# Optimization experiments

Hardware: AMD Instinct MI355X
Metric: run time of the kernel (lower is better)

The kernel has to match this reference:

```python
import jax, jax.numpy as jnp
import numpy as np

IMAGE_MAX_DIM = 1024
POOL = 7
NUM_CLASSES = 81
N_ROIS = 2000
BN_EPS = 1e-3


def _make_boxes(key, n):
    k1, k2, k3, k4 = jax.random.split(key, 4)
    cx = jax.random.uniform(k1, (n,), minval=0.0, maxval=IMAGE_MAX_DIM)
    cy = jax.random.uniform(k2, (n,), minval=0.0, maxval=IMAGE_MAX_DIM)
    w = jax.random.uniform(k3, (n,), minval=16.0, maxval=512.0)
    h = jax.random.uniform(k4, (n,), minval=16.0, maxval=512.0)
    x1 = jnp.clip(cx - w / 2, 0.0, IMAGE_MAX_DIM - 2.0)
    y1 = jnp.clip(cy - h / 2, 0.0, IMAGE_MAX_DIM - 2.0)
    x2 = jnp.clip(cx + w / 2, x1 + 1.0, IMAGE_MAX_DIM)
    y2 = jnp.clip(cy + h / 2, y1 + 1.0, IMAGE_MAX_DIM)
    return jnp.stack([x1, y1, x2, y2], axis=-1)[None]  # [1, n, 4]


def setup_inputs() -> dict:
    key = jax.random.key(0)
    ks = jax.random.split(key, 16)
    d = {
        'p2': jax.random.normal(ks[0], (1, 256, 256, 256), jnp.float32),
        'p3': jax.random.normal(ks[1], (1, 256, 128, 128), jnp.float32),
        'p4': jax.random.normal(ks[2], (1, 256, 64, 64), jnp.float32),
        'p5': jax.random.normal(ks[3], (1, 256, 32, 32), jnp.float32),
        'rpn_rois': _make_boxes(ks[4], N_ROIS),
        'conv1_w': jax.random.normal(ks[5], (1024, 256, POOL, POOL), jnp.float32) * 0.02,
        'conv1_b': jnp.zeros((1024,), jnp.float32),
        'bn1_g': jnp.ones((1024,), jnp.float32),
        'bn1_b': jnp.zeros((1024,), jnp.float32),
        'bn1_m': jnp.zeros((1024,), jnp.float32),
        'bn1_v': jnp.ones((1024,), jnp.float32),
        'conv2_w': jax.random.normal(ks[6], (1024, 1024), jnp.float32) * 0.02,
        'conv2_b': jnp.zeros((1024,), jnp.float32),
        'bn2_g': jnp.ones((1024,), jnp.float32),
        'bn2_b': jnp.zeros((1024,), jnp.float32),
        'bn2_m': jnp.zeros((1024,), jnp.float32),
        'bn2_v': jnp.ones((1024,), jnp.float32),
        'logits_w': jax.random.normal(ks[7], (NUM_CLASSES, 1024), jnp.float32) * 0.02,
        'logits_b': jnp.zeros((NUM_CLASSES,), jnp.float32),
        'bbox_w': jax.random.normal(ks[8], (NUM_CLASSES * 4, 1024), jnp.float32) * 0.02,
        'bbox_b': jnp.zeros((NUM_CLASSES * 4,), jnp.float32),
    }
    return d


def _crop_resize(fmap, boxes):
    """TF-style crop_and_resize, bilinear. fmap [C,H,W]; boxes [N,4] = (y1,x1,y2,x2) normalized."""
    C, H, W = fmap.shape
    dt = fmap.dtype
    y1, x1, y2, x2 = boxes[:, 0], boxes[:, 1], boxes[:, 2], boxes[:, 3]
    t = (jnp.arange(POOL, dtype=dt) / (POOL - 1))  # [P]
    ys = y1[:, None] * (H - 1) + t[None, :] * ((y2 - y1) * (H - 1))[:, None]  # [N,P]
    xs = x1[:, None] * (W - 1) + t[None, :] * ((x2 - x1) * (W - 1))[:, None]  # [N,P]
    y0 = jnp.floor(ys)
    x0 = jnp.floor(xs)
    ly = (ys - y0)[None, :, :, None]  # [1,N,P,1]
    lx = (xs - x0)[None, :, None, :]  # [1,N,1,P]
    y0i = jnp.clip(y0.astype(jnp.int32), 0, H - 1)
    y1i = jnp.clip(y0i + 1, 0, H - 1)
    x0i = jnp.clip(x0.astype(jnp.int32), 0, W - 1)
    x1i = jnp.clip(x0i + 1, 0, W - 1)

    def g(yi, xi):  # -> [C,N,P,P]
        return fmap[:, yi[:, :, None], xi[:, None, :]]

    out = (g(y0i, x0i) * (1 - ly) * (1 - lx) + g(y0i, x1i) * (1 - ly) * lx
           + g(y1i, x0i) * ly * (1 - lx) + g(y1i, x1i) * ly * lx)
    return jnp.transpose(out, (1, 0, 2, 3))  # [N,C,P,P]


def _forward(p2, p3, p4, p5, rpn_rois, conv1_w, conv1_b, bn1_g, bn1_b, bn1_m, bn1_v,
             conv2_w, conv2_b, bn2_g, bn2_b, bn2_m, bn2_v, logits_w, logits_b, bbox_w, bbox_b):
    rois = rpn_rois.reshape(-1, 4)  # [N,4] (x1,y1,x2,y2) in pixels
    x1, y1, x2, y2 = rois[:, 0], rois[:, 1], rois[:, 2], rois[:, 3]
    # level = clamp(round(log2(sqrt(area)/224)) + 4, 2, 5)
    roi_level = jnp.clip(jnp.round(jnp.log2(jnp.sqrt((y2 - y1) * (x2 - x1)) / 224.0)) + 4.0, 2.0, 5.0)
    boxes_n = (rois / float(IMAGE_MAX_DIM))[:, [1, 0, 3, 2]]  # (y1,x1,y2,x2) normalized

    pooled = jnp.zeros((rois.shape[0], 256, POOL, POOL), rois.dtype)
    for lvl, fmap in zip(range(2, 6), [p2, p3, p4, p5]):
        crops = _crop_resize(fmap[0], boxes_n)  # [N,256,P,P]
        mask = (roi_level == float(lvl))[:, None, None, None]
        pooled = pooled + jnp.where(mask, crops, 0.0)

    # conv1: 7x7 valid conv over [N,256,7,7] -> [N,1024]
    h = jnp.einsum('nchw,ochw->no', pooled, conv1_w) + conv1_b
    h = (h - bn1_m) * jax.lax.rsqrt(bn1_v + BN_EPS) * bn1_g + bn1_b
    h = jax.nn.relu(h)
    # conv2: 1x1 conv == matmul
    h = h @ conv2_w.T + conv2_b
    h = (h - bn2_m) * jax.lax.rsqrt(bn2_v + BN_EPS) * bn2_g + bn2_b
    shared = jax.nn.relu(h)  # [N,1024]

    logits = shared @ logits_w.T + logits_b
    probs = jax.nn.softmax(logits, axis=-1)
    bbox = shared @ bbox_w.T + bbox_b
    return (logits.reshape(1, N_ROIS, NUM_CLASSES),
            probs.reshape(1, N_ROIS, NUM_CLASSES),
            bbox.reshape(1, N_ROIS, NUM_CLASSES, 4))


def reference(p2, p3, p4, p5, rpn_rois, conv1_w, conv1_b, bn1_g, bn1_b, bn1_m, bn1_v,
              conv2_w, conv2_b, bn2_g, bn2_b, bn2_m, bn2_v, logits_w, logits_b, bbox_w, bbox_b):
    return _forward(p2, p3, p4, p5, rpn_rois, conv1_w, conv1_b, bn1_g, bn1_b, bn1_m, bn1_v,
                    conv2_w, conv2_b, bn2_g, bn2_b, bn2_m, bn2_v, logits_w, logits_b, bbox_w, bbox_b)
```

## Files before the change

### kernel.cpp

```cpp
#include <hip/hip_runtime.h>
#include <stdint.h>

#define NROI 2000
#define MPAD 2048
#define KP   12544
#define N1   1024
#define NCLS 81
#define NBOX 324
#define N3   405
#define N3P  448
#define BN_EPS 0.001f
#define KSPLIT 8

typedef __attribute__((ext_vector_type(8))) short bf16x8;
typedef __attribute__((ext_vector_type(4))) float f32x4;
typedef __attribute__((ext_vector_type(8))) unsigned short u16x8;

__device__ inline unsigned short f2bf(float f) {
  union { float f; unsigned u; } v; v.f = f;
  unsigned r = v.u + 0x7fffu + ((v.u >> 16) & 1u);
  return (unsigned short)(r >> 16);
}

__device__ inline float bf2f(unsigned short h) {
  union { unsigned u; float f; } v; v.u = (unsigned)h << 16; return v.f;
}

__device__ inline void gld16(const unsigned short* g, unsigned short* l) {
  __builtin_amdgcn_global_load_lds(
      (const __attribute__((address_space(1))) void*)g,
      (__attribute__((address_space(3))) void*)l, 16, 0, 0);
}

__device__ __forceinline__ void kslice(int kz, int& off, int& len) {
  if (kz < 4) { off = kz * 1536; len = 1536; }
  else        { off = 6144 + (kz - 4) * 1600; len = 1600; }
}

__global__ __launch_bounds__(256) void front_t(
    const float* __restrict__ p2, const float* __restrict__ p3,
    const float* __restrict__ p4, const float* __restrict__ p5,
    unsigned short* __restrict__ f2t, unsigned short* __restrict__ f3t,
    unsigned short* __restrict__ f4t, unsigned short* __restrict__ f5t) {
  int bb2 = blockIdx.x;
  int t = threadIdx.x;
  const float* src;
  unsigned short* dst;
  int HW;
  if (bb2 < 1024)      { src = p2; dst = f2t; HW = 65536; }
  else if (bb2 < 1280) { bb2 -= 1024; src = p3; dst = f3t; HW = 16384; }
  else if (bb2 < 1344) { bb2 -= 1280; src = p4; dst = f4t; HW = 4096; }
  else                 { bb2 -= 1344; src = p5; dst = f5t; HW = 1024; }
  int p0 = bb2 * 64;
  int lane = t & 63, w = t >> 6;
  int pq = (lane & 15) * 4;
  int cg = (lane >> 4) * 8;
#pragma unroll
  for (int it = 0; it < 2; ++it) {
    int c = w * 64 + it * 32 + cg;
    const float* sp = src + (size_t)c * HW + p0 + pq;
    float4 v[8];
#pragma unroll
    for (int k = 0; k < 8; ++k)
      v[k] = *(const float4*)(sp + (size_t)k * HW);
    unsigned short* dp = dst + (size_t)(p0 + pq) * 256 + c;
    u16x8 o0, o1, o2, o3;
#pragma unroll
    for (int k = 0; k < 8; ++k) {
      o0[k] = f2bf(v[k].x);
      o1[k] = f2bf(v[k].y);
      o2[k] = f2bf(v[k].z);
      o3[k] = f2bf(v[k].w);
    }
    *(u16x8*)(dp)       = o0;
    *(u16x8*)(dp + 256) = o1;
    *(u16x8*)(dp + 512) = o2;
    *(u16x8*)(dp + 768) = o3;
  }
}

__global__ __launch_bounds__(256) void roi_prep(
    const unsigned short* __restrict__ f2t, const unsigned short* __restrict__ f3t,
    const unsigned short* __restrict__ f4t, const unsigned short* __restrict__ f5t,
    const float* __restrict__ rois, unsigned short* __restrict__ pooled,
    const float* __restrict__ c1w, const float* __restrict__ c2w,
    const float* __restrict__ lw, const float* __restrict__ bw,
    const float* c1b, const float* g1, const float* b1, const float* m1, const float* v1,
    const float* c2b, const float* g2, const float* b2, const float* m2, const float* v2,
    const float* lb, const float* bb,
    unsigned short* __restrict__ w1p, unsigned short* __restrict__ w2b,
    unsigned short* __restrict__ w3b,
    float* s1, float* t1, float* s2, float* t2, float* b3) {
  __shared__ unsigned short srep[6272];
  int b = blockIdx.x;
  int t = threadIdx.x;
  if (b < 2048) {
    int n = b;
    int lane = t & 63, w = t >> 6;
    int c0 = lane * 4;
    unsigned short* out = pooled + (size_t)n * KP;
    if (n >= NROI) {
      for (int p = w; p < 49; p += 4)
        *(ushort4*)(out + p * 256 + c0) = make_ushort4(0, 0, 0, 0);
      return;
    }
    float x1 = rois[n * 4 + 0], y1 = rois[n * 4 + 1];
    float x2 = rois[n * 4 + 2], y2 = rois[n * 4 + 3];
    float area = (y2 - y1) * (x2 - x1);
    float lvl_f = rintf(log2f(sqrtf(area) / 224.0f)) + 4.0f;
    lvl_f = fminf(fmaxf(lvl_f, 2.0f), 5.0f);
    int lvl = (int)lvl_f;
    const unsigned short* f;
    int H;
    if (lvl == 2)      { f = f2t; H = 256; }
    else if (lvl == 3) { f = f3t; H = 128; }
    else if (lvl == 4) { f = f4t; H = 64;  }
    else               { f = f5t; H = 32;  }
    int W = H;
    const float inv = 1.0f / 1024.0f;
    float yn1 = y1 * inv, xn1 = x1 * inv, yn2 = y2 * inv, xn2 = x2 * inv;
    float hs = (yn2 - yn1) * (H - 1);
    float ws = (xn2 - xn1) * (W - 1);
    float yb = yn1 * (H - 1);
    float xb = xn1 * (W - 1);

    for (int p = w; p < 49; p += 4) {
      int py = p / 7, px = p - py * 7;
      float ysv = yb + ((float)py / 6.0f) * hs;
      float xsv = xb + ((float)px / 6.0f) * ws;
      float y0f = floorf(ysv), x0f = floorf(xsv);
      float ly = ysv - y0f, lx = xsv - x0f;
      int y0 = min(max((int)y0f, 0), H - 1);
      int y1i = min(y0 + 1, H - 1);
      int x0 = min(max((int)x0f, 0), W - 1);
      int x1i = min(x0 + 1, W - 1);
      ushort4 v00 = *(const ushort4*)(f + ((size_t)y0 * W + x0) * 256 + c0);
      ushort4 v01 = *(const ushort4*)(f + ((size_t)y0 * W + x1i) * 256 + c0);
      ushort4 v10 = *(const ushort4*)(f + ((size_t)y1i * W + x0) * 256 + c0);
      ushort4 v11 = *(const ushort4*)(f + ((size_t)y1i * W + x1i) * 256 + c0);
      ushort4 o;
      {
        float a = bf2f(v00.x), bq = bf2f(v01.x), cq = bf2f(v10.x), d = bf2f(v11.x);
        float top = a + lx * (bq - a), bot = cq + lx * (d - cq);
        o.x = f2bf(top + ly * (bot - top));
      }
      {
        float a = bf2f(v00.y), bq = bf2f(v01.y), cq = bf2f(v10.y), d = bf2f(v11.y);
        float top = a + lx * (bq - a), bot = cq + lx * (d - cq);
        o.y = f2bf(top + ly * (bot - top));
      }
      {
        float a = bf2f(v00.z), bq = bf2f(v01.z), cq = bf2f(v10.z), d = bf2f(v11.z);
        float top = a + lx * (bq - a), bot = cq + lx * (d - cq);
        o.z = f2bf(top + ly * (bot - top));
      }
      {
        float a = bf2f(v00.w), bq = bf2f(v01.w), cq = bf2f(v10.w), d = bf2f(v11.w);
        float top = a + lx * (bq - a), bot = cq + lx * (d - cq);
        o.w = f2bf(top + ly * (bot - top));
      }
      *(ushort4*)(out + p * 256 + c0) = o;
    }
  } else if (b < 4096) {
    int idx = b - 2048;
    int o = idx >> 1, h = idx & 1;
    const float4* src = (const float4*)(c1w + (size_t)o * KP + h * 6272);
    for (int k = t; k < 1568; k += 256) {
      float4 v = src[k];
      ushort4 q;
      q.x = f2bf(v.x); q.y = f2bf(v.y); q.z = f2bf(v.z); q.w = f2bf(v.w);
      *(ushort4*)&srep[k * 4] = q;
    }
    __syncthreads();
    unsigned short* dst = w1p + (size_t)o * KP + h * 128;
    int ch4 = (t & 31) * 4;
    int jw = t >> 5;
    for (int j = jw; j < 49; j += 8) {
      ushort4 q;
      q.x = srep[(ch4 + 0) * 49 + j];
      q.y = srep[(ch4 + 1) * 49 + j];
      q.z = srep[(ch4 + 2) * 49 + j];
      q.w = srep[(ch4 + 3) * 49 + j];
      *(ushort4*)(dst + j * 256 + ch4) = q;
    }
  } else if (b < 5120) {
    int j4 = (b - 4096) * 256 + t;
    float4 v = ((const float4*)c2w)[j4];
    ushort4 q;
    q.x = f2bf(v.x); q.y = f2bf(v.y); q.z = f2bf(v.z); q.w = f2bf(v.w);
    *(ushort4*)(w2b + (size_t)j4 * 4) = q;
  } else if (b < 5568) {
    int row = b - 5120;
    int k = t * 4;
    float4 v = {0.f, 0.f, 0.f, 0.f};
    if (row < NCLS)      v = *(const float4*)(lw + (size_t)row * 1024 + k);
    else if (row < N3)   v = *(const float4*)(bw + (size_t)(row - NCLS) * 1024 + k);
    ushort4 q;
    q.x = f2bf(v.x); q.y = f2bf(v.y); q.z = f2bf(v.z); q.w = f2bf(v.w);
    *(ushort4*)(w3b + (size_t)row * 1024 + k) = q;
  } else {
    for (int i = t; i < 1024; i += 256) {
      float sc = g1[i] * rsqrtf(v1[i] + BN_EPS);
      s1[i] = sc;
      t1[i] = (c1b[i] - m1[i]) * sc + b1[i];
      float ss = g2[i] * rsqrtf(v2[i] + BN_EPS);
      s2[i] = ss;
      t2[i] = (c2b[i] - m2[i]) * ss + b2[i];
    }
    for (int i = t; i < N3P; i += 256)
      b3[i] = (i < NCLS) ? lb[i] : (i < N3 ? bb[i - NCLS] : 0.0f);
  }
}

__global__ __launch_bounds__(512, 2) void gemm1_sk2(
    const unsigned short* __restrict__ A, const unsigned short* __restrict__ B,
    unsigned short* __restrict__ part) {
  __shared__ unsigned short AsF[4 * 8192];
  __shared__ unsigned short BsF[4 * 8192];
  int bid = blockIdx.x;
  int kz = bid & 7;
  int u = bid >> 3;
  int bn0 = (u & 3) * 256;
  int bm0 = (u >> 2) * 256;
  int koff, klen;
  kslice(kz, koff, klen);
  int nt = klen >> 6;

  int t = threadIdx.x;
  int lane = t & 63, w = t >> 6;
  int wr = w >> 2, wc = w & 3;
  int ln = lane & 15, q = lane >> 4;

  int clog = (lane & 3) ^ ((lane >> 3) & 3);
  int l4 = lane >> 2;
  const unsigned short* gA0 = A + (size_t)(bm0 + w * 32 + l4) * KP + koff + clog * 8;
  const unsigned short* gA1 = gA0 + (size_t)16 * KP;
  const unsigned short* gB0 = B + (size_t)(bn0 + w * 32 + l4) * KP + koff + clog * 8;
  const unsigned short* gB1 = gB0 + (size_t)16 * KP;
  int dc0 = (w * 128 + lane) * 8;
  int dc1 = dc0 + 64 * 8;

  int rxor = (q ^ ((ln >> 1) & 3)) * 8;
  int rdA = (wr * 128 + ln) * 32 + rxor;
  int rdB = (wc * 64 + ln) * 32 + rxor;

  f32x4 acc[8][4] = {};

#pragma unroll
  for (int kk = 0; kk < 2; ++kk) {
    int src = kk * 32;
    int db = kk * 8192;
    gld16(gA0 + src, AsF + db + dc0);
    gld16(gA1 + src, AsF + db + dc1);
    gld16(gB0 + src, BsF + db + dc0);
    gld16(gB1 + src, BsF + db + dc1);
  }
  asm volatile("s_waitcnt vmcnt(4)" ::: "memory");
  __builtin_amdgcn_s_barrier();
  asm volatile("" ::: "memory");

  for (int tt = 0; tt < nt; ++tt) {
    int slot = tt & 1;
    int nslot = slot ^ 1;
    int knext = (tt + 1 < nt) ? (tt + 1) * 64 : 0;
#pragma unroll
    for (int kk = 0; kk < 2; ++kk) {
      int rb = (slot * 2 + kk) * 8192;
      bf16x8 af[8], bfr[4];
#pragma unroll
      for (int mi = 0; mi < 8; ++mi)
        af[mi] = *(const bf16x8*)&AsF[rb + rdA + mi * 512];
#pragma unroll
      for (int nj = 0; nj < 4; ++nj)
        bfr[nj] = *(const bf16x8*)&BsF[rb + rdB + nj * 512];

      int src = knext + kk * 32;
      int db = (nslot * 2 + kk) * 8192;
      gld16(gA0 + src, AsF + db + dc0);
      gld16(gA1 + src, AsF + db + dc1);
      gld16(gB0 + src, BsF + db + dc0);
      gld16(gB1 + src, BsF + db + dc1);

      asm volatile("s_waitcnt vmcnt(4)" ::: "memory");
      __builtin_amdgcn_s_barrier();
      asm volatile("" ::: "memory");

      __builtin_amdgcn_s_setprio(1);
#pragma unroll
      for (int mi = 0; mi < 8; ++mi)
#pragma unroll
        for (int nj = 0; nj < 4; ++nj)
          acc[mi][nj] = __builtin_amdgcn_mfma_f32_16x16x32_bf16(
              af[mi], bfr[nj], acc[mi][nj], 0, 0, 0);
      __builtin_amdgcn_s_setprio(0);

      asm volatile("" ::: "memory");
      __builtin_amdgcn_s_barrier();
      asm volatile("" ::: "memory");
    }
  }

  unsigned short* po = part + (size_t)kz * MPAD * N1;
#pragma unroll
  for (int mi = 0; mi < 8; ++mi) {
    int m = bm0 + wr * 128 + mi * 16 + q * 4;
#pragma unroll
    for (int nj = 0; nj < 4; ++nj) {
      int n = bn0 + wc * 64 + nj * 16 + ln;
#pragma unroll
      for (int r = 0; r < 4; ++r)
        po[(size_t)(m + r) * N1 + n] = f2bf(acc[mi][nj][r]);
    }
  }
}

__global__ void reduce_sk(const unsigned short* __restrict__ part,
                          const float* __restrict__ sc, const float* __restrict__ sh,
                          unsigned short* __restrict__ outb) {
  const size_t P = (size_t)MPAD * N1;
  int m = blockIdx.x;
  int t = threadIdx.x;
  float4 v = {0.f, 0.f, 0.f, 0.f};
#pragma unroll
  for (int kz = 0; kz < KSPLIT; ++kz) {
    ushort4 u = *(const ushort4*)(part + kz * P + (size_t)m * N1 + t * 4);
    v.x += bf2f(u.x); v.y += bf2f(u.y); v.z += bf2f(u.z); v.w += bf2f(u.w);
  }
  int n0 = t * 4;
  ushort4 o;
  if (m < NROI) {
    o.x = f2bf(fmaxf(v.x * sc[n0 + 0] + sh[n0 + 0], 0.0f));
    o.y = f2bf(fmaxf(v.y * sc[n0 + 1] + sh[n0 + 1], 0.0f));
    o.z = f2bf(fmaxf(v.z * sc[n0 + 2] + sh[n0 + 2], 0.0f));
    o.w = f2bf(fmaxf(v.w * sc[n0 + 3] + sh[n0 + 3], 0.0f));
  } else {
    o = make_ushort4(0, 0, 0, 0);
  }
  *(ushort4*)(outb + (size_t)m * N1 + n0) = o;
}

template <int MODE>
__global__ __launch_bounds__(256) void gemm_bt(
    const unsigned short* __restrict__ A, const unsigned short* __restrict__ B,
    int M, int N, int K,
    const float* __restrict__ sc, const float* __restrict__ sh,
    unsigned short* __restrict__ outb, float* __restrict__ outf,
    int validM, int ldo) {
  __shared__ unsigned short As[64 * 64];
  __shared__ unsigned short Bs[64 * 64];
  int bm0 = blockIdx.y * 64;
  int bn0 = blockIdx.x * 64;
  int t = threadIdx.x;
  int lane = t & 63, w = t >> 6;
  int wm = (w & 1) * 32, wn = (w >> 1) * 32;
  int ln = lane & 15, q = lane >> 4;

  int r8 = t >> 3, j8 = t & 7;
  int sj = j8 ^ (r8 & 7);
  const unsigned short* ga = A + (size_t)(bm0 + r8) * K + sj * 8;
  const unsigned short* gb = B + (size_t)(bn0 + r8) * K + sj * 8;
  unsigned short* la = &As[t * 8];
  unsigned short* lb = &Bs[t * 8];
  int e = ln & 7;

  f32x4 acc00 = {0.f, 0.f, 0.f, 0.f}, acc01 = {0.f, 0.f, 0.f, 0.f};
  f32x4 acc10 = {0.f, 0.f, 0.f, 0.f}, acc11 = {0.f, 0.f, 0.f, 0.f};

  for (int k0 = 0; k0 < K; k0 += 64) {
    gld16(ga + k0, la);
    gld16(ga + k0 + (size_t)32 * K, la + 2048);
    gld16(gb + k0, lb);
    gld16(gb + k0 + (size_t)32 * K, lb + 2048);
    __syncthreads();
#pragma unroll
    for (int h = 0; h < 2; ++h) {
      int slot = ((h * 4 + q) ^ e) * 8;
      bf16x8 a0 = *(const bf16x8*)&As[(wm + ln) * 64 + slot];
      bf16x8 a1 = *(const bf16x8*)&As[(wm + 16 + ln) * 64 + slot];
      bf16x8 b0 = *(const bf16x8*)&Bs[(wn + ln) * 64 + slot];
      bf16x8 b1 = *(const bf16x8*)&Bs[(wn + 16 + ln) * 64 + slot];
      acc00 = __builtin_amdgcn_mfma_f32_16x16x32_bf16(a0, b0, acc00, 0, 0, 0);
      acc01 = __builtin_amdgcn_mfma_f32_16x16x32_bf16(a0, b1, acc01, 0, 0, 0);
      acc10 = __builtin_amdgcn_mfma_f32_16x16x32_bf16(a1, b0, acc10, 0, 0, 0);
      acc11 = __builtin_amdgcn_mfma_f32_16x16x32_bf16(a1, b1, acc11, 0, 0, 0);
    }
    __syncthreads();
  }

  f32x4 accs[2][2] = {{acc00, acc01}, {acc10, acc11}};
#pragma unroll
  for (int i = 0; i < 2; ++i)
#pragma unroll
    for (int j = 0; j < 2; ++j)
#pragma unroll
      for (int r = 0; r < 4; ++r) {
        int m = bm0 + wm + i * 16 + q * 4 + r;
        int n = bn0 + wn + j * 16 + ln;
        float v = accs[i][j][r];
        if (MODE == 1) {
          float o = fmaxf(v * sc[n] + sh[n], 0.0f);
          outb[(size_t)m * ldo + n] = (m < validM) ? f2bf(o) : (unsigned short)0;
        } else {
          outf[(size_t)m * ldo + n] = v + sh[n];
        }
      }
}

__global__ void head(const float* __restrict__ fc3, float* __restrict__ out) {
  int r = blockIdx.x;
  int t = threadIdx.x;
  const float* row = fc3 + (size_t)r * N3P;
  float v0 = (t < NCLS) ? row[t] : -INFINITY;
  float v1 = (t + 64 < NCLS) ? row[t + 64] : -INFINITY;
  float m = fmaxf(v0, v1);
#pragma unroll
  for (int o = 32; o > 0; o >>= 1) m = fmaxf(m, __shfl_xor(m, o, 64));
  float e0 = (t < NCLS) ? expf(v0 - m) : 0.0f;
  float e1 = (t + 64 < NCLS) ? expf(v1 - m) : 0.0f;
  float s = e0 + e1;
#pragma unroll
  for (int o = 32; o > 0; o >>= 1) s += __shfl_xor(s, o, 64);
  float invs = 1.0f / s;
  float* ol = out + (size_t)r * NCLS;
  float* op = out + 162000 + (size_t)r * NCLS;
  float* ob = out + 324000 + (size_t)r * NBOX;
  if (t < NCLS) { ol[t] = v0; op[t] = e0 * invs; }
  if (t + 64 < NCLS) { ol[t + 64] = v1; op[t + 64] = e1 * invs; }
  for (int j = t; j < NBOX; j += 64) ob[j] = row[NCLS + j];
}

extern "C" void kernel_launch(void* const* d_in, const int* in_sizes, int n_in,
                              void* d_out, int out_size, void* d_ws, size_t ws_size,
                              hipStream_t stream) {
  const float* p2  = (const float*)d_in[0];
  const float* p3  = (const float*)d_in[1];
  const float* p4  = (const float*)d_in[2];
  const float* p5  = (const float*)d_in[3];
  const float* roi = (const float*)d_in[4];
  const float* c1w = (const float*)d_in[5];
  const float* c1b = (const float*)d_in[6];
  const float* g1  = (const float*)d_in[7];
  const float* b1  = (const float*)d_in[8];
  const float* m1  = (const float*)d_in[9];
  const float* v1  = (const float*)d_in[10];
  const float* c2w = (const float*)d_in[11];
  const float* c2b = (const float*)d_in[12];
  const float* g2  = (const float*)d_in[13];
  const float* b2  = (const float*)d_in[14];
  const float* m2  = (const float*)d_in[15];
  const float* v2  = (const float*)d_in[16];
  const float* lw  = (const float*)d_in[17];
  const float* lb  = (const float*)d_in[18];
  const float* bw  = (const float*)d_in[19];
  const float* bb  = (const float*)d_in[20];
  float* out = (float*)d_out;

  char* ws = (char*)d_ws;
  size_t off = 0;
  auto alloc = [&](size_t bytes) {
    void* p = ws + off;
    off = (off + bytes + 255) & ~(size_t)255;
    return p;
  };
  unsigned short* pooled = (unsigned short*)alloc((size_t)MPAD * KP * 2);
  unsigned short* w1p    = (unsigned short*)alloc((size_t)N1 * KP * 2);
  unsigned short* w2b    = (unsigned short*)alloc((size_t)N1 * N1 * 2);
  unsigned short* w3b    = (unsigned short*)alloc((size_t)N3P * N1 * 2);
  unsigned short* a2     = (unsigned short*)alloc((size_t)MPAD * N1 * 2);
  unsigned short* shd    = (unsigned short*)alloc((size_t)MPAD * N1 * 2);
  float* fc3 = (float*)alloc((size_t)MPAD * N3P * 4);
  char* ub = (char*)alloc((size_t)48 * 1024 * 1024);
  unsigned short* f2t = (unsigned short*)ub;
  unsigned short* f3t = (unsigned short*)(ub + 33554432);
  unsigned short* f4t = (unsigned short*)(ub + 33554432 + 8388608);
  unsigned short* f5t = (unsigned short*)(ub + 33554432 + 8388608 + 2097152);
  unsigned short* part = (unsigned short*)ub;
  float* s1  = (float*)alloc(1024 * 4);
  float* t1  = (float*)alloc(1024 * 4);
  float* s2  = (float*)alloc(1024 * 4);
  float* t2  = (float*)alloc(1024 * 4);
  float* b3  = (float*)alloc(N3P * 4);

  front_t<<<1360, 256, 0, stream>>>(p2, p3, p4, p5, f2t, f3t, f4t, f5t);

  roi_prep<<<5569, 256, 0, stream>>>(f2t, f3t, f4t, f5t, roi, pooled,
                                     c1w, c2w, lw, bw,
                                     c1b, g1, b1, m1, v1, c2b, g2, b2, m2, v2,
                                     lb, bb,
                                     w1p, w2b, w3b, s1, t1, s2, t2, b3);

  gemm1_sk2<<<256, 512, 0, stream>>>(pooled, w1p, part);
  reduce_sk<<<MPAD, 256, 0, stream>>>(part, s1, t1, a2);

  gemm_bt<1><<<dim3(N1 / 64, MPAD / 64), 256, 0, stream>>>(
      a2, w2b, MPAD, N1, N1, s2, t2, shd, nullptr, NROI, N1);
  gemm_bt<2><<<dim3(N3P / 64, MPAD / 64), 256, 0, stream>>>(
      shd, w3b, MPAD, N3P, N1, nullptr, b3, nullptr, fc3, NROI, N3P);

  head<<<NROI, 64, 0, stream>>>(fc3, out);
}
```

Measured before the change: 315.4 us.

## Restructure split-K GEMM1 into a 4-slot, 3-deep async load ring

Replaces the double-buffered two-halves-per-iteration loop with a 4-slot ring of 32-wide K phases. Three loads stay in flight, and there is a single wait plus barrier per phase instead of two barriers per half-step. The goal is to hide global-to-LDS latency better and cut synchronisation per MFMA batch in the dominant GEMM. There is a risk of a WAR hazard: slot (ph+3)&3 is written while other waves may still be reading slot ph-1, and only one barrier separates the phases.

```diff
diff --git a/kernel.cpp b/kernel.cpp
--- a/kernel.cpp
+++ b/kernel.cpp
@@ -212,7 +212,7 @@
   }
 }
 
-__global__ __launch_bounds__(512, 2) void gemm1_sk2(
+__global__ __launch_bounds__(512, 2) void gemm1_sk3(
     const unsigned short* __restrict__ A, const unsigned short* __restrict__ B,
     unsigned short* __restrict__ part) {
   __shared__ unsigned short AsF[4 * 8192];
@@ -224,7 +224,7 @@
   int bm0 = (u >> 2) * 256;
   int koff, klen;
   kslice(kz, koff, klen);
-  int nt = klen >> 6;
+  int nph = klen >> 5;
 
   int t = threadIdx.x;
   int lane = t & 63, w = t >> 6;
@@ -247,58 +247,51 @@
   f32x4 acc[8][4] = {};
 
 #pragma unroll
-  for (int kk = 0; kk < 2; ++kk) {
-    int src = kk * 32;
-    int db = kk * 8192;
+  for (int ph = 0; ph < 3; ++ph) {
+    int src = ph * 32;
+    int db = ph * 8192;
     gld16(gA0 + src, AsF + db + dc0);
     gld16(gA1 + src, AsF + db + dc1);
     gld16(gB0 + src, BsF + db + dc0);
     gld16(gB1 + src, BsF + db + dc1);
   }
-  asm volatile("s_waitcnt vmcnt(4)" ::: "memory");
+  asm volatile("s_waitcnt vmcnt(8)" ::: "memory");
   __builtin_amdgcn_s_barrier();
   asm volatile("" ::: "memory");
 
-  for (int tt = 0; tt < nt; ++tt) {
-    int slot = tt & 1;
-    int nslot = slot ^ 1;
-    int knext = (tt + 1 < nt) ? (tt + 1) * 64 : 0;
-#pragma unroll
-    for (int kk = 0; kk < 2; ++kk) {
-      int rb = (slot * 2 + kk) * 8192;
-      bf16x8 af[8], bfr[4];
-#pragma unroll
-      for (int mi = 0; mi < 8; ++mi)
-        af[mi] = *(const bf16x8*)&AsF[rb + rdA + mi * 512];
+  for (int ph = 0; ph < nph; ++ph) {
+    int rb = (ph & 3) * 8192;
+    bf16x8 af[8], bfr[4];
+#pragma unroll
+    for (int mi = 0; mi < 8; ++mi)
+      af[mi] = *(const bf16x8*)&AsF[rb + rdA + mi * 512];
+#pragma unroll
+    for (int nj = 0; nj < 4; ++nj)
+      bfr[nj] = *(const bf16x8*)&BsF[rb + rdB + nj * 512];
+
+    int phn = ph + 3;
+    int src = (phn < nph) ? phn * 32 : 0;
+    int db = (phn & 3) * 8192;
+    gld16(gA0 + src, AsF + db + dc0);
+    gld16(gA1 + src, AsF + db + dc1);
+    gld16(gB0 + src, BsF + db + dc0);
+    gld16(gB1 + src, BsF + db + dc1);
+
+    __builtin_amdgcn_s_setprio(1);
+#pragma unroll
+    for (int mi = 0; mi < 8; ++mi)
 #pragma unroll
       for (int nj = 0; nj < 4; ++nj)
-        bfr[nj] = *(const bf16x8*)&BsF[rb + rdB + nj * 512];
-
-      int src = knext + kk * 32;
-      int db = (nslot * 2 + kk) * 8192;
-      gld16(gA0 + src, AsF + db + dc0);
-      gld16(gA1 + src, AsF + db + dc1);
-      gld16(gB0 + src, BsF + db + dc0);
-      gld16(gB1 + src, BsF + db + dc1);
-
-      asm volatile("s_waitcnt vmcnt(4)" ::: "memory");
-      __builtin_amdgcn_s_barrier();
-      asm volatile("" ::: "memory");
-
-      __builtin_amdgcn_s_setprio(1);
-#pragma unroll
-      for (int mi = 0; mi < 8; ++mi)
-#pragma unroll
-        for (int nj = 0; nj < 4; ++nj)
-          acc[mi][nj] = __builtin_amdgcn_mfma_f32_16x16x32_bf16(
-              af[mi], bfr[nj], acc[mi][nj], 0, 0, 0);
-      __builtin_amdgcn_s_setprio(0);
-
-      asm volatile("" ::: "memory");
-      __builtin_amdgcn_s_barrier();
-      asm volatile("" ::: "memory");
-    }
-  }
+        acc[mi][nj] = __builtin_amdgcn_mfma_f32_16x16x32_bf16(
+            af[mi], bfr[nj], acc[mi][nj], 0, 0, 0);
+    __builtin_amdgcn_s_setprio(0);
+
+    asm volatile("s_waitcnt vmcnt(8)" ::: "memory");
+    __builtin_amdgcn_s_barrier();
+    asm volatile("" ::: "memory");
+  }
+
+  asm volatile("s_waitcnt vmcnt(0)" ::: "memory");
 
   unsigned short* po = part + (size_t)kz * MPAD * N1;
 #pragma unroll
@@ -489,7 +482,7 @@
                                      lb, bb,
                                      w1p, w2b, w3b, s1, t1, s2, t2, b3);
 
-  gemm1_sk2<<<256, 512, 0, stream>>>(pooled, w1p, part);
+  gemm1_sk3<<<256, 512, 0, stream>>>(pooled, w1p, part);
   reduce_sk<<<MPAD, 256, 0, stream>>>(part, s1, t1, a2);
 
   gemm_bt<1><<<dim3(N1 / 64, MPAD / 64), 256, 0, stream>>>(
```

Result: no change. 309.7 us (-1.8%).

## Split gemm1 k-step into four interleaved load/MFMA phases

Applied to the files above, without the earlier changes.

Restructures the main split-K GEMM loop so that each 32-wide k sub-step is split into two half-M MFMA phases. A-tile and B-tile global-to-LDS loads are issued separately between those phases, and register fragments are loaded in smaller groups. The goal is to overlap global loads, LDS reads and MFMA work more finely and lower register pressure from holding 8 A fragments at once. It changes the barrier and waitcnt placement, which risks LDS hazards or extra synchronisation stalls.

```diff
diff --git a/kernel.cpp b/kernel.cpp
--- a/kernel.cpp
+++ b/kernel.cpp
@@ -212,7 +212,7 @@
   }
 }
 
-__global__ __launch_bounds__(512, 2) void gemm1_sk2(
+__global__ __launch_bounds__(512, 2) void gemm1_sk6(
     const unsigned short* __restrict__ A, const unsigned short* __restrict__ B,
     unsigned short* __restrict__ part) {
   __shared__ unsigned short AsF[4 * 8192];
@@ -246,15 +246,14 @@
 
   f32x4 acc[8][4] = {};
 
-#pragma unroll
-  for (int kk = 0; kk < 2; ++kk) {
-    int src = kk * 32;
-    int db = kk * 8192;
-    gld16(gA0 + src, AsF + db + dc0);
-    gld16(gA1 + src, AsF + db + dc1);
-    gld16(gB0 + src, BsF + db + dc0);
-    gld16(gB1 + src, BsF + db + dc1);
-  }
+  gld16(gA0 + 0,  AsF + 0 * 8192 + dc0);
+  gld16(gA1 + 0,  AsF + 0 * 8192 + dc1);
+  gld16(gB0 + 0,  BsF + 0 * 8192 + dc0);
+  gld16(gB1 + 0,  BsF + 0 * 8192 + dc1);
+  gld16(gA0 + 32, AsF + 1 * 8192 + dc0);
+  gld16(gA1 + 32, AsF + 1 * 8192 + dc1);
+  gld16(gB0 + 32, BsF + 1 * 8192 + dc0);
+  gld16(gB1 + 32, BsF + 1 * 8192 + dc1);
   asm volatile("s_waitcnt vmcnt(4)" ::: "memory");
   __builtin_amdgcn_s_barrier();
   asm volatile("" ::: "memory");
@@ -263,42 +262,86 @@
     int slot = tt & 1;
     int nslot = slot ^ 1;
     int knext = (tt + 1 < nt) ? (tt + 1) * 64 : 0;
-#pragma unroll
-    for (int kk = 0; kk < 2; ++kk) {
-      int rb = (slot * 2 + kk) * 8192;
-      bf16x8 af[8], bfr[4];
-#pragma unroll
-      for (int mi = 0; mi < 8; ++mi)
-        af[mi] = *(const bf16x8*)&AsF[rb + rdA + mi * 512];
+    int rb0 = (slot * 2 + 0) * 8192;
+    int rb1 = (slot * 2 + 1) * 8192;
+    int db0 = (nslot * 2 + 0) * 8192;
+    int db1 = (nslot * 2 + 1) * 8192;
+    bf16x8 afl[4], afh[4], bfr[4];
+
+#pragma unroll
+    for (int mi = 0; mi < 4; ++mi)
+      afl[mi] = *(const bf16x8*)&AsF[rb0 + rdA + mi * 512];
+#pragma unroll
+    for (int nj = 0; nj < 4; ++nj)
+      bfr[nj] = *(const bf16x8*)&BsF[rb0 + rdB + nj * 512];
+    gld16(gA0 + knext, AsF + db0 + dc0);
+    gld16(gA1 + knext, AsF + db0 + dc1);
+    __builtin_amdgcn_s_barrier();
+    asm volatile("" ::: "memory");
+    __builtin_amdgcn_s_setprio(1);
+#pragma unroll
+    for (int mi = 0; mi < 4; ++mi)
 #pragma unroll
       for (int nj = 0; nj < 4; ++nj)
-        bfr[nj] = *(const bf16x8*)&BsF[rb + rdB + nj * 512];
-
-      int src = knext + kk * 32;
-      int db = (nslot * 2 + kk) * 8192;
-      gld16(gA0 + src, AsF + db + dc0);
-      gld16(gA1 + src, AsF + db + dc1);
-      gld16(gB0 + src, BsF + db + dc0);
-      gld16(gB1 + src, BsF + db + dc1);
-
-      asm volatile("s_waitcnt vmcnt(4)" ::: "memory");
-      __builtin_amdgcn_s_barrier();
-      asm volatile("" ::: "memory");
-
-      __builtin_amdgcn_s_setprio(1);
-#pragma unroll
-      for (int mi = 0; mi < 8; ++mi)
-#pragma unroll
-        for (int nj = 0; nj < 4; ++nj)
-          acc[mi][nj] = __builtin_amdgcn_mfma_f32_16x16x32_bf16(
-              af[mi], bfr[nj], acc[mi][nj], 0, 0, 0);
-      __builtin_amdgcn_s_setprio(0);
-
-      asm volatile("" ::: "memory");
-      __builtin_amdgcn_s_barrier();
-      asm volatile("" ::: "memory");
-    }
-  }
+        acc[mi][nj] = __builtin_amdgcn_mfma_f32_16x16x32_bf16(
+            afl[mi], bfr[nj], acc[mi][nj], 0, 0, 0);
+    __builtin_amdgcn_s_setprio(0);
+
+#pragma unroll
+    for (int mi = 0; mi < 4; ++mi)
+      afh[mi] = *(const bf16x8*)&AsF[rb0 + rdA + (mi + 4) * 512];
+    gld16(gB0 + knext, BsF + db0 + dc0);
+    gld16(gB1 + knext, BsF + db0 + dc1);
+    asm volatile("s_waitcnt vmcnt(4)" ::: "memory");
+    __builtin_amdgcn_s_barrier();
+    asm volatile("" ::: "memory");
+    __builtin_amdgcn_s_setprio(1);
+#pragma unroll
+    for (int mi = 0; mi < 4; ++mi)
+#pragma unroll
+      for (int nj = 0; nj < 4; ++nj)
+        acc[mi + 4][nj] = __builtin_amdgcn_mfma_f32_16x16x32_bf16(
+            afh[mi], bfr[nj], acc[mi + 4][nj], 0, 0, 0);
+    __builtin_amdgcn_s_setprio(0);
+
+#pragma unroll
+    for (int mi = 0; mi < 4; ++mi)
+      afl[mi] = *(const bf16x8*)&AsF[rb1 + rdA + mi * 512];
+#pragma unroll
+    for (int nj = 0; nj < 4; ++nj)
+      bfr[nj] = *(const bf16x8*)&BsF[rb1 + rdB + nj * 512];
+    gld16(gA0 + knext + 32, AsF + db1 + dc0);
+    gld16(gA1 + knext + 32, AsF + db1 + dc1);
+    __builtin_amdgcn_s_barrier();
+    asm volatile("" ::: "memory");
+    __builtin_amdgcn_s_setprio(1);
+#pragma unroll
+    for (int mi = 0; mi < 4; ++mi)
+#pragma unroll
+      for (int nj = 0; nj < 4; ++nj)
+        acc[mi][nj] = __builtin_amdgcn_mfma_f32_16x16x32_bf16(
+            afl[mi], bfr[nj], acc[mi][nj], 0, 0, 0);
+    __builtin_amdgcn_s_setprio(0);
+
+#pragma unroll
+    for (int mi = 0; mi < 4; ++mi)
+      afh[mi] = *(const bf16x8*)&AsF[rb1 + rdA + (mi + 4) * 512];
+    gld16(gB0 + knext + 32, BsF + db1 + dc0);
+    gld16(gB1 + knext + 32, BsF + db1 + dc1);
+    asm volatile("s_waitcnt vmcnt(4)" ::: "memory");
+    __builtin_amdgcn_s_barrier();
+    asm volatile("" ::: "memory");
+    __builtin_amdgcn_s_setprio(1);
+#pragma unroll
+    for (int mi = 0; mi < 4; ++mi)
+#pragma unroll
+      for (int nj = 0; nj < 4; ++nj)
+        acc[mi + 4][nj] = __builtin_amdgcn_mfma_f32_16x16x32_bf16(
+            afh[mi], bfr[nj], acc[mi + 4][nj], 0, 0, 0);
+    __builtin_amdgcn_s_setprio(0);
+  }
+
+  asm volatile("s_waitcnt vmcnt(0)" ::: "memory");
 
   unsigned short* po = part + (size_t)kz * MPAD * N1;
 #pragma unroll
@@ -489,7 +532,7 @@
                                      lb, bb,
                                      w1p, w2b, w3b, s1, t1, s2, t2, b3);
 
-  gemm1_sk2<<<256, 512, 0, stream>>>(pooled, w1p, part);
+  gemm1_sk6<<<256, 512, 0, stream>>>(pooled, w1p, part);
   reduce_sk<<<MPAD, 256, 0, stream>>>(part, s1, t1, a2);
 
   gemm_bt<1><<<dim3(N1 / 64, MPAD / 64), 256, 0, stream>>>(
```

Result: no change. 321.5 us (+1.9%).
